# Kernel optimization log

Hardware: AMD Instinct MI355X
Metric: run time of the kernel (lower is better)

## Reference

```python
import jax, jax.numpy as jnp
import numpy as np
from jax import lax

EPS = 1e-6  # LayerNorm2d eps


def _ln2d(x, w, b):
    # channel-wise LayerNorm over dim 1 of [B,C,H,W]
    mu = jnp.mean(x, axis=1, keepdims=True)
    var = jnp.mean((x - mu) ** 2, axis=1, keepdims=True)
    return (x - mu) / jnp.sqrt(var + EPS) * w[None, :, None, None] + b[None, :, None, None]


def _conv1x1(x, w, b):
    # w: [O, C]
    return jnp.einsum('bchw,oc->bohw', x, w) + b[None, :, None, None]


def _dconv(x, w, b):
    # 3x3 conv, dilation 4, padding 4 -> same H,W. w: [O, C, 3, 3]
    y = lax.conv_general_dilated(x, w, window_strides=(1, 1),
                                 padding=((4, 4), (4, 4)), rhs_dilation=(4, 4),
                                 dimension_numbers=('NCHW', 'OIHW', 'NCHW'))
    return y + b[None, :, None, None]


def _forward(x_l, x_r, nl_w, nl_b, nr_w, nr_b, lp1_w, lp1_b, rp1_w, rp1_b,
             dl_w, dl_b, dr_w, dr_b, lp2_w, lp2_b, rp2_w, rp2_b, beta, gamma):
    c = x_l.shape[1]
    scale = c ** (-0.5)
    N_l = _ln2d(x_l, nl_w, nl_b)
    N_r = _ln2d(x_r, nr_w, nr_b)
    V_l = jnp.transpose(_conv1x1(x_l, lp2_w, lp2_b), (0, 2, 3, 1))   # [B,H,W,C]
    V_r = jnp.transpose(_conv1x1(x_r, rp2_w, rp2_b), (0, 2, 3, 1))
    Q_l = jnp.transpose(_conv1x1(N_l, lp1_w, lp1_b), (0, 2, 3, 1))   # [B,H,W,C]
    Q_r = jnp.transpose(_conv1x1(N_r, rp1_w, rp1_b), (0, 2, 3, 1))
    K_l_T = jnp.transpose(_dconv(N_l, dl_w, dl_b), (0, 2, 1, 3))     # [B,H,C,W]
    K_r_T = jnp.transpose(_dconv(N_r, dr_w, dr_b), (0, 2, 1, 3))
    # per-row cross attention: [B,H,W,W]
    attn_r2l = jnp.einsum('bhwc,bhcv->bhwv', Q_l, K_r_T) * scale
    attn_l2r = jnp.einsum('bhwc,bhcv->bhwv', Q_r, K_l_T) * scale
    F_r2l = jnp.einsum('bhwv,bhvc->bhwc', jax.nn.softmax(attn_r2l, axis=-1), V_r)
    F_l2r = jnp.einsum('bhwv,bhvc->bhwc', jax.nn.softmax(attn_l2r, axis=-1), V_l)
    F_r2l = jnp.transpose(F_r2l, (0, 3, 1, 2)) * beta   # [B,C,H,W]
    F_l2r = jnp.transpose(F_l2r, (0, 3, 1, 2)) * gamma
    return x_l + F_r2l, x_r + F_l2r


def setup_inputs() -> dict:
    key = jax.random.key(0)
    ks = jax.random.split(key, 12)
    B, C, H, W = 2, 128, 192, 512
    s = 0.02
    rn = lambda k, shp: s * jax.random.normal(k, shp, jnp.float32)
    return {
        'x_l': jax.random.normal(ks[0], (B, C, H, W), jnp.float32),
        'x_r': jax.random.normal(ks[1], (B, C, H, W), jnp.float32),
        'nl_w': jnp.ones((C,), jnp.float32), 'nl_b': jnp.zeros((C,), jnp.float32),
        'nr_w': jnp.ones((C,), jnp.float32), 'nr_b': jnp.zeros((C,), jnp.float32),
        'lp1_w': rn(ks[2], (C, C)), 'lp1_b': jnp.zeros((C,), jnp.float32),
        'rp1_w': rn(ks[3], (C, C)), 'rp1_b': jnp.zeros((C,), jnp.float32),
        'dl_w': rn(ks[4], (C, C, 3, 3)), 'dl_b': jnp.zeros((C,), jnp.float32),
        'dr_w': rn(ks[5], (C, C, 3, 3)), 'dr_b': jnp.zeros((C,), jnp.float32),
        'lp2_w': rn(ks[6], (C, C)), 'lp2_b': jnp.zeros((C,), jnp.float32),
        'rp2_w': rn(ks[7], (C, C)), 'rp2_b': jnp.zeros((C,), jnp.float32),
        'beta': 0.1 * jax.random.normal(ks[8], (1, C, 1, 1), jnp.float32),
        'gamma': 0.1 * jax.random.normal(ks[9], (1, C, 1, 1), jnp.float32),
    }


def reference(x_l, x_r, nl_w, nl_b, nr_w, nr_b, lp1_w, lp1_b, rp1_w, rp1_b,
              dl_w, dl_b, dr_w, dr_b, lp2_w, lp2_b, rp2_w, rp2_b, beta, gamma):
    return _forward(x_l, x_r, nl_w, nl_b, nr_w, nr_b, lp1_w, lp1_b, rp1_w, rp1_b,
                    dl_w, dl_b, dr_w, dr_b, lp2_w, lp2_b, rp2_w, rp2_b, beta, gamma)
```

## Files before the change

### kernel.cpp

```cpp
#include <hip/hip_runtime.h>
#include <stdint.h>

#define CC 128
#define HH 192
#define WW 512
#define BB 2
#define HW (HH*WW)
#define CHW (CC*HW)
#define TENS (BB*CHW)

typedef __attribute__((ext_vector_type(8))) short bf16x8;
typedef __attribute__((ext_vector_type(4))) short bf16x4;
typedef __attribute__((ext_vector_type(4))) float f32x4;

__device__ __forceinline__ unsigned short f2bf(float f) {
    union { float f; unsigned u; } v; v.f = f;
    return (unsigned short)((v.u + 0x7FFFu + ((v.u >> 16) & 1u)) >> 16);
}
__device__ __forceinline__ float bf2f(unsigned short u) {
    union { unsigned u; float f; } v; v.u = ((unsigned)u) << 16;
    return v.f;
}
__device__ __forceinline__ uint32_t cvtpk(float lo, float hi) {
    uint32_t r;
    asm("v_cvt_pk_bf16_f32 %0, %1, %2" : "=v"(r) : "v"(lo), "v"(hi));
    return r;
}
__device__ __forceinline__ f32x4 MFMA(bf16x8 a, bf16x8 b, f32x4 c) {
    return __builtin_amdgcn_mfma_f32_16x16x32_bf16(a, b, c, 0, 0, 0);
}
__device__ __forceinline__ f32x4 MFMA16(bf16x4 a, bf16x4 b, f32x4 c) {
#if __has_builtin(__builtin_amdgcn_mfma_f32_16x16x16_bf16)
    return __builtin_amdgcn_mfma_f32_16x16x16_bf16(a, b, c, 0, 0, 0);
#elif __has_builtin(__builtin_amdgcn_mfma_f32_16x16x16bf16_1k)
    return __builtin_amdgcn_mfma_f32_16x16x16bf16_1k(a, b, c, 0, 0, 0);
#else
    f32x4 d = c;
    asm("v_mfma_f32_16x16x16_bf16 %0, %1, %2, %0" : "+v"(d) : "v"(a), "v"(b));
    return d;
#endif
}
__device__ __forceinline__ void gload_lds16(const void* g, void* l) {
    __builtin_amdgcn_global_load_lds(
        (const __attribute__((address_space(1))) void*)g,
        (__attribute__((address_space(3))) void*)l, 16, 0, 0);
}

__global__ __launch_bounds__(256) void wcast_k(
    const float* __restrict__ dlw, const float* __restrict__ drw,
    unsigned short* __restrict__ wd)
{
    int i = blockIdx.x * 256 + threadIdx.x;
    if (i >= 2 * 9 * CC * CC) return;
    int e  = i & 7;
    int l  = (i >> 3) & 63;
    int n_ = (i >> 9) & 3;
    int kk = (i >> 11) & 3;
    int oh = (i >> 13) & 1;
    int rest = i >> 14;
    int tap = rest % 9;
    int side = rest / 9;
    int o = oh * 64 + n_ * 16 + (l & 15);
    int c = kk * 32 + (l >> 4) * 8 + e;
    const float* src = side ? drw : dlw;
    wd[i] = f2bf(src[((size_t)o * CC + c) * 9 + tap]);
}

__global__ __launch_bounds__(256) void lnv_k(
    const float* __restrict__ xl, const float* __restrict__ xr,
    const float* __restrict__ nlw, const float* __restrict__ nlb,
    const float* __restrict__ nrw, const float* __restrict__ nrb,
    const float* __restrict__ wlp, const float* __restrict__ blp,
    const float* __restrict__ wrp, const float* __restrict__ brp,
    unsigned short* __restrict__ ntl, unsigned short* __restrict__ ntr,
    unsigned short* __restrict__ vlo, unsigned short* __restrict__ vro)
{
    const int side = blockIdx.y;
    const float* x  = side ? xr : xl;
    const float* nw = side ? nrw : nlw;
    const float* nb = side ? nrb : nlb;
    const float* wv = side ? wrp : wlp;
    const float* bv = side ? brp : blp;
    unsigned short* nt = side ? ntr : ntl;
    unsigned short* vo = side ? vro : vlo;
    const int bid = blockIdx.x;
    const int wt = bid & 7, h = (bid >> 3) % HH, b = bid / (8 * HH);
    const int w0 = wt * 64;
    const int t = threadIdx.x;

    __shared__ unsigned short sA[64][136];
    __shared__ unsigned short sB[128][136];
    __shared__ float red[8][64];
    __shared__ float smu[64], srs[64];

    {
        const int w = t & 63, cg = t >> 6;
        const float* xp = x + (size_t)b * CHW + (size_t)h * WW + w0 + w;
        float s = 0.f, q = 0.f;
        for (int i = 0; i < 16; i++) {
            int c = cg * 32 + i * 2;
            float v0 = xp[(size_t)c * HW];
            float v1 = xp[(size_t)(c + 1) * HW];
            *(uint32_t*)&sA[w][c] = cvtpk(v0, v1);
            s += v0 + v1; q += v0 * v0 + v1 * v1;
        }
        red[cg][w] = s; red[4 + cg][w] = q;
    }
    for (int it = 0; it < 16; it++) {
        int f = it * 1024 + t * 4;
        int o = f >> 7, c = f & 127;
        float4 v = *(const float4*)(wv + o * CC + c);
        *(uint32_t*)&sB[o][c]     = cvtpk(v.x, v.y);
        *(uint32_t*)&sB[o][c + 2] = cvtpk(v.z, v.w);
    }
    __syncthreads();
    if (t < 64) {
        float S = red[0][t] + red[1][t] + red[2][t] + red[3][t];
        float Q = red[4][t] + red[5][t] + red[6][t] + red[7][t];
        float mu = S * (1.f / CC);
        float var = fmaxf(Q * (1.f / CC) - mu * mu, 0.f);
        smu[t] = mu; srs[t] = rsqrtf(var + 1e-6f);
    }
    __syncthreads();
    {
        const int cl = (t & 63) * 2, wg = t >> 6;
        const float nwa = nw[cl], nwb = nw[cl + 1];
        const float nba = nb[cl], nbb = nb[cl + 1];
        unsigned short* npb = nt + ((size_t)(b * HH + h) * WW + w0) * CC;
        for (int wp = 0; wp < 16; wp++) {
            int w = wp * 4 + wg;
            float mu = smu[w], rs = srs[w];
            float v0 = (bf2f(sA[w][cl]) - mu) * rs * nwa + nba;
            float v1 = (bf2f(sA[w][cl + 1]) - mu) * rs * nwb + nbb;
            *(uint32_t*)&npb[(size_t)w * CC + cl] = cvtpk(v0, v1);
        }
    }
    const int wid = t >> 6, l = t & 63, lr = l & 15, lg = l >> 4;
    f32x4 acc[8] = {};
    for (int kk = 0; kk < 4; kk++) {
        bf16x8 a = *(const bf16x8*)&sA[wid * 16 + lr][kk * 32 + lg * 8];
#pragma unroll
        for (int n_ = 0; n_ < 8; n_++) {
            bf16x8 bb = *(const bf16x8*)&sB[n_ * 16 + lr][kk * 32 + lg * 8];
            acc[n_] = MFMA(a, bb, acc[n_]);
        }
    }
    unsigned short* vp = vo + ((size_t)(b * HH + h) * CC) * WW + w0;
    for (int n_ = 0; n_ < 8; n_++) {
        int o = n_ * 16 + lr;
        float bias = bv[o];
        uint2 uu;
        uu.x = cvtpk(acc[n_][0] + bias, acc[n_][1] + bias);
        uu.y = cvtpk(acc[n_][2] + bias, acc[n_][3] + bias);
        *(uint2*)&vp[(size_t)o * WW + wid * 16 + lg * 4] = uu;
    }
}

__global__ __launch_bounds__(256) void dconv_k(
    const unsigned short* __restrict__ ntl, const unsigned short* __restrict__ ntr,
    const unsigned short* __restrict__ wfr,
    const float* __restrict__ dlb, const float* __restrict__ drb,
    unsigned short* __restrict__ klo, unsigned short* __restrict__ kro)
{
    const int side = blockIdx.y;
    const unsigned short* nt = side ? ntr : ntl;
    const unsigned short* wbase = wfr + (size_t)side * 9 * 16384;
    const float* bd = side ? drb : dlb;
    unsigned short* ko = side ? kro : klo;
    const int bid0 = blockIdx.x;
    const int lgc = (bid0 & 7) * 192 + (bid0 >> 3);
    const int wt = lgc & 3;
    const int hb = lgc >> 2;
    const int h = hb % HH, b = hb / HH;
    const int w0 = wt * 128;
    const int t = threadIdx.x;
    const int wid = t >> 6, l = t & 63, lr = l & 15, lg = l >> 4;
    const int whalf = wid & 1, ohalf = wid >> 1;

    __shared__ unsigned short sA[136][136];

    f32x4 acc[4][4] = {};
    for (int dy = 0; dy < 3; dy++) {
        const int hh = h + 4 * (dy - 1);
        const bool hok = (hh >= 0 && hh < HH);
        __syncthreads();
        for (int f = t * 8; f < 136 * 128; f += 2048) {
            int wloc = f >> 7, c = f & 127;
            int w = w0 - 4 + wloc;
            bf16x8 v = {0, 0, 0, 0, 0, 0, 0, 0};
            if (hok && w >= 0 && w < WW)
                v = *(const bf16x8*)(nt + ((size_t)(b * HH + hh) * WW + w) * CC + c);
            *(bf16x8*)&sA[wloc][c] = v;
        }
        __syncthreads();
#pragma unroll
        for (int dx = 0; dx < 3; dx++) {
            const unsigned short* wtap =
                wbase + (size_t)(dy * 3 + dx) * 16384 + ohalf * 8192 + l * 8;
#pragma unroll
            for (int kk = 0; kk < 4; kk++) {
                bf16x8 bfr[4];
#pragma unroll
                for (int n_ = 0; n_ < 4; n_++)
                    bfr[n_] = *(const bf16x8*)(wtap + (kk * 4 + n_) * 512);
                bf16x8 af[4];
#pragma unroll
                for (int g = 0; g < 4; g++)
                    af[g] = *(const bf16x8*)&sA[whalf * 64 + g * 16 + lr + 4 * dx][kk * 32 + lg * 8];
#pragma unroll
                for (int g = 0; g < 4; g++)
#pragma unroll
                    for (int n_ = 0; n_ < 4; n_++)
                        acc[g][n_] = MFMA(af[g], bfr[n_], acc[g][n_]);
            }
        }
    }
    unsigned short* kp = ko + ((size_t)(b * HH + h) * WW + w0) * CC;
    for (int g = 0; g < 4; g++)
        for (int n_ = 0; n_ < 4; n_++) {
            int o = ohalf * 64 + n_ * 16 + lr;
            float bias = bd[o];
            for (int j = 0; j < 4; j++) {
                int w = whalf * 64 + g * 16 + lg * 4 + j;
                kp[(size_t)w * CC + o] = f2bf(acc[g][n_][j] + bias);
            }
        }
}

__global__ __launch_bounds__(256, 2) void attn_k(
    const unsigned short* __restrict__ ntl, const unsigned short* __restrict__ ntr,
    const unsigned short* __restrict__ kl,  const unsigned short* __restrict__ kr,
    const unsigned short* __restrict__ vtl, const unsigned short* __restrict__ vtr,
    const float* __restrict__ lp1w, const float* __restrict__ lp1b,
    const float* __restrict__ rp1w, const float* __restrict__ rp1b,
    const float* __restrict__ xl, const float* __restrict__ xr,
    const float* __restrict__ beta, const float* __restrict__ gamma,
    float* __restrict__ out)
{
    __shared__ __align__(16) char smem[65536];
    unsigned short* sWh = (unsigned short*)(smem + 32768);

    const int dir = blockIdx.z;
    const unsigned short* nq  = dir ? ntr : ntl;
    const unsigned short* kws = dir ? kl : kr;
    const unsigned short* vws = dir ? vtl : vtr;
    const float* wq   = dir ? rp1w : lp1w;
    const float* bq   = dir ? rp1b : lp1b;
    const float* xres = dir ? xr : xl;
    const float* mult = dir ? gamma : beta;
    float* op = out + (size_t)dir * TENS;

    const int bid = blockIdx.x;
    const int xcd = bid & 7;
    const int s   = bid >> 3;
    const int qb  = s & 3;
    const int bh  = xcd + 8 * (s >> 2);
    const int q0  = qb * 128;
    const int t = threadIdx.x;
    const int wid = t >> 6, l = t & 63, lr = l & 15, lg = l >> 4;

    const unsigned short* ksrc = kws + (size_t)bh * WW * CC;
    const unsigned short* vsrc = vws + (size_t)bh * CC * WW;

    int koff[4], voff[4];
    {
        int rl = wid * 4 + (l >> 4);
        int gci = (l & 15) ^ rl;
#pragma unroll
        for (int it = 0; it < 4; it++)
            koff[it] = (it * 16 + rl) * CC + gci * 8;
    }
#pragma unroll
    for (int it = 0; it < 4; it++) {
        int row = it * 32 + wid * 8 + (l >> 3);
        int gci = (l & 7) ^ (row & 7);
        voff[it] = row * WW + gci * 8;
    }

#pragma unroll
    for (int it = 0; it < 4; it++)
        gload_lds16(ksrc + koff[it], smem + it * 4096 + wid * 1024);
#pragma unroll
    for (int it = 0; it < 4; it++)
        gload_lds16(vsrc + voff[it], smem + 16384 + it * 4096 + wid * 1024);

    bf16x8 nf[2][4];
    {
        const unsigned short* nsrc = nq + ((size_t)bh * WW + q0) * CC;
#pragma unroll
        for (int qg = 0; qg < 2; qg++)
#pragma unroll
            for (int kk = 0; kk < 4; kk++)
                nf[qg][kk] = *(const bf16x8*)(nsrc + (wid * 32 + qg * 16 + lr) * CC
                                              + kk * 32 + lg * 8);
    }

    const float SCL = 0.08838834764831845f * 1.4426950408889634f;
    bf16x8 qf[4][2];
    const int srcA = lr + ((l & 16) << 1);
    const int srcB = srcA + 16;
    const int hi = lg >> 1;
    uint32_t ew[2][2];
#pragma unroll
    for (int h_ = 0; h_ < 2; h_++) {
        if (h_) __syncthreads();
        for (int it = 0; it < 8; it++) {
            int f = it * 1024 + t * 4;
            int o = f >> 7, c = f & 127;
            float4 v = *(const float4*)(wq + (h_ * 64 + o) * CC + c);
            *(uint32_t*)&sWh[o * 136 + c]     = cvtpk(v.x, v.y);
            *(uint32_t*)&sWh[o * 136 + c + 2] = cvtpk(v.z, v.w);
        }
        __syncthreads();
#pragma unroll
        for (int n4 = 0; n4 < 4; n4++) {
            bf16x8 wqA[4];
#pragma unroll
            for (int kk = 0; kk < 4; kk++)
                wqA[kk] = *(const bf16x8*)&sWh[(n4 * 16 + lr) * 136 + kk * 32 + lg * 8];
            f32x4 qa0 = {}, qa1 = {};
#pragma unroll
            for (int kk = 0; kk < 4; kk++) {
                qa0 = MFMA(wqA[kk], nf[0][kk], qa0);
                qa1 = MFMA(wqA[kk], nf[1][kk], qa1);
            }
            float4 b4 = *(const float4*)(bq + h_ * 64 + n4 * 16 + lg * 4);
            uint32_t w0q0 = cvtpk((qa0[0] + b4.x) * SCL, (qa0[1] + b4.y) * SCL);
            uint32_t w1q0 = cvtpk((qa0[2] + b4.z) * SCL, (qa0[3] + b4.w) * SCL);
            uint32_t w0q1 = cvtpk((qa1[0] + b4.x) * SCL, (qa1[1] + b4.y) * SCL);
            uint32_t w1q1 = cvtpk((qa1[2] + b4.z) * SCL, (qa1[3] + b4.w) * SCL);
            if (!(n4 & 1)) {
                ew[0][0] = w0q0; ew[0][1] = w1q0;
                ew[1][0] = w0q1; ew[1][1] = w1q1;
            } else {
                const int s_ = h_ * 2 + (n4 >> 1);
                const uint32_t ow00 = w0q0, ow01 = w1q0, ow10 = w0q1, ow11 = w1q1;
                {
                    uint32_t e0A = __shfl((int)ew[0][0], srcA, 64);
                    uint32_t e1A = __shfl((int)ew[0][1], srcA, 64);
                    uint32_t o0A = __shfl((int)ow00, srcA, 64);
                    uint32_t o1A = __shfl((int)ow01, srcA, 64);
                    uint32_t e0B = __shfl((int)ew[0][0], srcB, 64);
                    uint32_t e1B = __shfl((int)ew[0][1], srcB, 64);
                    uint32_t o0B = __shfl((int)ow00, srcB, 64);
                    uint32_t o1B = __shfl((int)ow01, srcB, 64);
                    union { uint32_t u[4]; bf16x8 v; } f;
                    f.u[0] = hi ? o0A : e0A;
                    f.u[1] = hi ? o1A : e1A;
                    f.u[2] = hi ? o0B : e0B;
                    f.u[3] = hi ? o1B : e1B;
                    qf[s_][0] = f.v;
                }
                {
                    uint32_t e0A = __shfl((int)ew[1][0], srcA, 64);
                    uint32_t e1A = __shfl((int)ew[1][1], srcA, 64);
                    uint32_t o0A = __shfl((int)ow10, srcA, 64);
                    uint32_t o1A = __shfl((int)ow11, srcA, 64);
                    uint32_t e0B = __shfl((int)ew[1][0], srcB, 64);
                    uint32_t e1B = __shfl((int)ew[1][1], srcB, 64);
                    uint32_t o0B = __shfl((int)ow10, srcB, 64);
                    uint32_t o1B = __shfl((int)ow11, srcB, 64);
                    union { uint32_t u[4]; bf16x8 v; } f;
                    f.u[0] = hi ? o0A : e0A;
                    f.u[1] = hi ? o1A : e1A;
                    f.u[2] = hi ? o0B : e0B;
                    f.u[3] = hi ? o1B : e1B;
                    qf[s_][1] = f.v;
                }
            }
        }
    }

    f32x4 oacc[8][2] = {};
    float lrow[2] = {0.f, 0.f};
    const int lr7 = lr & 7;

    for (int kb = 0; kb < 8; kb++) {
        const int base = (kb & 1) << 15;
        __syncthreads();
        if (kb < 7) {
            const int nbase = ((kb + 1) & 1) << 15;
            const unsigned short* kS = ksrc + (kb + 1) * 64 * CC;
            const unsigned short* vS = vsrc + (kb + 1) * 64;
#pragma unroll
            for (int it = 0; it < 4; it++)
                gload_lds16(kS + koff[it], smem + nbase + it * 4096 + wid * 1024);
#pragma unroll
            for (int it = 0; it < 4; it++)
                gload_lds16(vS + voff[it], smem + nbase + 16384 + it * 4096 + wid * 1024);
        }
        f32x4 sacc[2][4] = {};
        __builtin_amdgcn_s_setprio(1);
#pragma unroll
        for (int kk = 0; kk < 4; kk++)
#pragma unroll
            for (int n_ = 0; n_ < 4; n_++) {
                bf16x8 kf = *(const bf16x8*)(smem + base + (n_ * 16 + lr) * 256
                                             + (((kk * 4 + lg) ^ lr) << 4));
                sacc[0][n_] = MFMA(kf, qf[kk][0], sacc[0][n_]);
                sacc[1][n_] = MFMA(kf, qf[kk][1], sacc[1][n_]);
            }
        __builtin_amdgcn_s_setprio(0);
#pragma unroll
        for (int qg = 0; qg < 2; qg++) {
            float rs = 0.f;
#pragma unroll
            for (int n_ = 0; n_ < 4; n_++)
#pragma unroll
                for (int j = 0; j < 4; j++) {
                    float e = exp2f(sacc[qg][n_][j]);
                    sacc[qg][n_][j] = e;
                    rs += e;
                }
            rs += __shfl_xor(rs, 16, 64);
            rs += __shfl_xor(rs, 32, 64);
            lrow[qg] += rs;
        }
        __builtin_amdgcn_s_setprio(1);
#pragma unroll
        for (int n_ = 0; n_ < 4; n_++) {
            union { uint32_t u[2]; bf16x4 v; } b0, b1;
            b0.u[0] = cvtpk(sacc[0][n_][0], sacc[0][n_][1]);
            b0.u[1] = cvtpk(sacc[0][n_][2], sacc[0][n_][3]);
            b1.u[0] = cvtpk(sacc[1][n_][0], sacc[1][n_][1]);
            b1.u[1] = cvtpk(sacc[1][n_][2], sacc[1][n_][3]);
#pragma unroll
            for (int n8 = 0; n8 < 8; n8++) {
                bf16x4 va = *(const bf16x4*)(smem + base + 16384 + (n8 * 16 + lr) * 128
                                             + ((((n_ * 2) + (lg >> 1)) ^ lr7) << 4)
                                             + ((lg & 1) << 3));
                oacc[n8][0] = MFMA16(va, b0.v, oacc[n8][0]);
                oacc[n8][1] = MFMA16(va, b1.v, oacc[n8][1]);
            }
        }
        __builtin_amdgcn_s_setprio(0);
    }

    const float inv0 = 1.f / lrow[0], inv1 = 1.f / lrow[1];
    const int b = bh / HH, h = bh % HH;
    const int w_0 = q0 + wid * 32 + lr;
    const float* xp0 = xres + (size_t)b * CHW + (size_t)h * WW + w_0;
    float* outp0 = op + (size_t)b * CHW + (size_t)h * WW + w_0;
#pragma unroll
    for (int n_ = 0; n_ < 8; n_++) {
        float4 m4 = *(const float4*)&mult[n_ * 16 + lg * 4];
#pragma unroll
        for (int j = 0; j < 4; j++) {
            int c = n_ * 16 + lg * 4 + j;
            float mj = (&m4.x)[j];
            outp0[(size_t)c * HW]      = xp0[(size_t)c * HW]      + oacc[n_][0][j] * inv0 * mj;
            outp0[(size_t)c * HW + 16] = xp0[(size_t)c * HW + 16] + oacc[n_][1][j] * inv1 * mj;
        }
    }
}

extern "C" void kernel_launch(void* const* d_in, const int* in_sizes, int n_in,
                              void* d_out, int out_size, void* d_ws, size_t ws_size,
                              hipStream_t stream)
{
    const float* xl   = (const float*)d_in[0];
    const float* xr   = (const float*)d_in[1];
    const float* nlw  = (const float*)d_in[2];
    const float* nlb  = (const float*)d_in[3];
    const float* nrw  = (const float*)d_in[4];
    const float* nrb  = (const float*)d_in[5];
    const float* lp1w = (const float*)d_in[6];
    const float* lp1b = (const float*)d_in[7];
    const float* rp1w = (const float*)d_in[8];
    const float* rp1b = (const float*)d_in[9];
    const float* dlw  = (const float*)d_in[10];
    const float* dlb  = (const float*)d_in[11];
    const float* drw  = (const float*)d_in[12];
    const float* drb  = (const float*)d_in[13];
    const float* lp2w = (const float*)d_in[14];
    const float* lp2b = (const float*)d_in[15];
    const float* rp2w = (const float*)d_in[16];
    const float* rp2b = (const float*)d_in[17];
    const float* beta = (const float*)d_in[18];
    const float* gamma= (const float*)d_in[19];
    float* out = (float*)d_out;

    unsigned short* ws = (unsigned short*)d_ws;
    const size_t A = (size_t)TENS;
    unsigned short* Ntl = ws;
    unsigned short* Ntr = ws + A;
    unsigned short* Kl  = ws + 2 * A;
    unsigned short* Kr  = ws + 3 * A;
    unsigned short* Vtl = ws + 4 * A;
    unsigned short* Vtr = ws + 5 * A;
    unsigned short* Wd  = ws + 6 * A;

    wcast_k<<<dim3(1152), 256, 0, stream>>>(dlw, drw, Wd);
    lnv_k<<<dim3(3072, 2), 256, 0, stream>>>(xl, xr, nlw, nlb, nrw, nrb,
        lp2w, lp2b, rp2w, rp2b, Ntl, Ntr, Vtl, Vtr);
    dconv_k<<<dim3(1536, 2), 256, 0, stream>>>(Ntl, Ntr, Wd, dlb, drb, Kl, Kr);
    attn_k<<<dim3(1536, 1, 2), 256, 0, stream>>>(Ntl, Ntr, Kl, Kr, Vtl, Vtr,
        lp1w, lp1b, rp1w, rp1b, xl, xr, beta, gamma, out);
}
```

Before: 487.2 us.

## Stage dconv output through LDS and compute softmax row sums with MFMA

The dilated-conv kernel now writes its bias-added bf16 results into shared memory and then copies them to global memory with coalesced 16-byte stores. Before, each thread wrote scattered 2-byte stores. In the attention kernel, the per-row softmax denominator is now an extra MFMA against a ones vector instead of scalar adds plus cross-lane shuffles. This uses bf16-rounded probabilities, matching what feeds the PV product. The trade-offs are two extra barriers and reuse of sA in the conv epilogue, plus two added MFMAs per n_ step in the attention loop.

```diff
diff --git a/kernel.cpp b/kernel.cpp
--- a/kernel.cpp
+++ b/kernel.cpp
@@ -215,16 +215,25 @@
             }
         }
     }
-    unsigned short* kp = ko + ((size_t)(b * HH + h) * WW + w0) * CC;
+    __syncthreads();
     for (int g = 0; g < 4; g++)
         for (int n_ = 0; n_ < 4; n_++) {
             int o = ohalf * 64 + n_ * 16 + lr;
             float bias = bd[o];
+#pragma unroll
             for (int j = 0; j < 4; j++) {
                 int w = whalf * 64 + g * 16 + lg * 4 + j;
-                kp[(size_t)w * CC + o] = f2bf(acc[g][n_][j] + bias);
+                sA[w][o] = f2bf(acc[g][n_][j] + bias);
             }
         }
+    __syncthreads();
+    unsigned short* kp = ko + ((size_t)(b * HH + h) * WW + w0) * CC;
+#pragma unroll
+    for (int it = 0; it < 8; it++) {
+        int f = it * 2048 + t * 8;
+        int w = f >> 7, c = f & 127;
+        *(bf16x8*)&kp[(size_t)w * CC + c] = *(const bf16x8*)&sA[w][c];
+    }
 }
 
 __global__ __launch_bounds__(256, 2) void attn_k(
@@ -372,7 +381,8 @@
     }
 
     f32x4 oacc[8][2] = {};
-    float lrow[2] = {0.f, 0.f};
+    f32x4 osum[2] = {};
+    const bf16x4 ones = {(short)0x3F80, (short)0x3F80, (short)0x3F80, (short)0x3F80};
     const int lr7 = lr & 7;
 
     for (int kb = 0; kb < 8; kb++) {
@@ -402,20 +412,12 @@
             }
         __builtin_amdgcn_s_setprio(0);
 #pragma unroll
-        for (int qg = 0; qg < 2; qg++) {
-            float rs = 0.f;
+        for (int qg = 0; qg < 2; qg++)
 #pragma unroll
             for (int n_ = 0; n_ < 4; n_++)
 #pragma unroll
-                for (int j = 0; j < 4; j++) {
-                    float e = exp2f(sacc[qg][n_][j]);
-                    sacc[qg][n_][j] = e;
-                    rs += e;
-                }
-            rs += __shfl_xor(rs, 16, 64);
-            rs += __shfl_xor(rs, 32, 64);
-            lrow[qg] += rs;
-        }
+                for (int j = 0; j < 4; j++)
+                    sacc[qg][n_][j] = exp2f(sacc[qg][n_][j]);
         __builtin_amdgcn_s_setprio(1);
 #pragma unroll
         for (int n_ = 0; n_ < 4; n_++) {
@@ -424,6 +426,8 @@
             b0.u[1] = cvtpk(sacc[0][n_][2], sacc[0][n_][3]);
             b1.u[0] = cvtpk(sacc[1][n_][0], sacc[1][n_][1]);
             b1.u[1] = cvtpk(sacc[1][n_][2], sacc[1][n_][3]);
+            osum[0] = MFMA16(ones, b0.v, osum[0]);
+            osum[1] = MFMA16(ones, b1.v, osum[1]);
 #pragma unroll
             for (int n8 = 0; n8 < 8; n8++) {
                 bf16x4 va = *(const bf16x4*)(smem + base + 16384 + (n8 * 16 + lr) * 128
@@ -436,7 +440,7 @@
         __builtin_amdgcn_s_setprio(0);
     }
 
-    const float inv0 = 1.f / lrow[0], inv1 = 1.f / lrow[1];
+    const float inv0 = 1.f / osum[0][0], inv1 = 1.f / osum[1][0];
     const int b = bh / HH, h = bh % HH;
     const int w_0 = q0 + wid * 32 + lr;
     const float* xp0 = xres + (size_t)b * CHW + (size_t)h * WW + w_0;
```

New measurement: 487.1 us. Within noise of the previous version (-0.0%).
